# Optimization experiments

Hardware: AMD Instinct MI355X
Metric: run time of the kernel (lower is better)

The kernel has to match this reference:

```python
import jax, jax.numpy as jnp
import numpy as np

N_NODES = 100000
N_EDGES = 1600000
IN_CH = 128
HID = 128
OUT_CH = 16
N_GRAPHS = 64


def setup_inputs() -> dict:
    key = jax.random.key(0)
    ks = jax.random.split(key, 8)
    x = jax.random.normal(ks[0], (N_NODES, IN_CH), dtype=jnp.float32)
    edge_index = jax.random.randint(ks[1], (2, N_EDGES), 0, N_NODES, dtype=jnp.int64)
    batch = jnp.sort(jax.random.randint(ks[2], (N_NODES,), 0, N_GRAPHS, dtype=jnp.int64))
    s1 = 1.0 / np.sqrt(IN_CH)
    s2 = 1.0 / np.sqrt(HID)
    W1 = jax.random.uniform(ks[3], (IN_CH, HID), jnp.float32, -s1, s1)
    b1 = jnp.zeros((HID,), jnp.float32)
    W2 = jax.random.uniform(ks[4], (HID, HID), jnp.float32, -s2, s2)
    b2 = jnp.zeros((HID,), jnp.float32)
    Wfc = jax.random.uniform(ks[5], (HID, OUT_CH), jnp.float32, -s2, s2)
    bfc = jax.random.uniform(ks[6], (OUT_CH,), jnp.float32, -s2, s2)
    return {"x": x, "W1": W1, "b1": b1, "W2": W2, "b2": b2,
            "Wfc": Wfc, "bfc": bfc, "edge_index": edge_index, "batch": batch}


def _gcn_conv(x, W, b, src, dst, deg_inv_sqrt, deg_inv):
    # GCNConv with self-loops: out = D^-1/2 (A+I) D^-1/2 (x W) + b
    h = x @ W                                   # [N, H]
    norm = deg_inv_sqrt[src] * deg_inv_sqrt[dst]  # [E]
    agg = jax.ops.segment_sum(h[src] * norm[:, None], dst, num_segments=N_NODES)
    # self-loop term: deg_inv_sqrt[i]^2 * h[i]
    return agg + h * deg_inv[:, None] + b


def reference(x, W1, b1, W2, b2, Wfc, bfc, edge_index, batch):
    src, dst = edge_index[0], edge_index[1]
    # degree including self-loop
    deg = jax.ops.segment_sum(jnp.ones((N_EDGES,), jnp.float32), dst, num_segments=N_NODES) + 1.0
    deg_inv_sqrt = jax.lax.rsqrt(deg)
    deg_inv = 1.0 / deg
    h = jax.nn.relu(_gcn_conv(x, W1, b1, src, dst, deg_inv_sqrt, deg_inv))
    h = jax.nn.relu(_gcn_conv(h, W2, b2, src, dst, deg_inv_sqrt, deg_inv))
    # global mean pool over graphs
    sums = jax.ops.segment_sum(h, batch, num_segments=N_GRAPHS)          # [G, H]
    counts = jax.ops.segment_sum(jnp.ones((N_NODES,), jnp.float32), batch, num_segments=N_GRAPHS)
    pooled = sums / jnp.maximum(counts, 1.0)[:, None]
    return pooled @ Wfc + bfc
```

## Files before the change

kernel.cpp:

```cpp
#include <hip/hip_runtime.h>
#include <math.h>

#define NN 100000
#define NE 1600000
#define CH 128
#define OUTC 16
#define NG 64

#define CBSH 9
#define NCB 196
#define CHK 8192
#define MAXB 12288
#define PS 8

typedef __attribute__((ext_vector_type(8))) short bf16x8;
typedef __attribute__((ext_vector_type(4))) float f32x4;

__device__ __forceinline__ unsigned short f2bf(float f) {
    union { float f; unsigned u; } v; v.f = f;
    unsigned r = v.u + 0x7FFF + ((v.u >> 16) & 1);
    return (unsigned short)(r >> 16);
}
__device__ __forceinline__ float bflo(unsigned u) {
    union { unsigned u; float f; } v; v.u = u << 16; return v.f;
}
__device__ __forceinline__ float bfhi(unsigned u) {
    union { unsigned u; float f; } v; v.u = u & 0xffff0000u; return v.f;
}

__global__ void k_init0(int* __restrict__ bcnt) {
    int i = blockIdx.x * 256 + threadIdx.x;
    if (i < NCB) bcnt[i] = 0;
}

__global__ __launch_bounds__(1024) void k_hist(const int* __restrict__ dst, int* __restrict__ bcnt) {
    __shared__ int h[NCB];
    int t = threadIdx.x;
    if (t < NCB) h[t] = 0;
    __syncthreads();
    int base = blockIdx.x * CHK;
#pragma unroll
    for (int i = 0; i < 8; i++) {
        int e = base + i * 1024 + t;
        if (e < NE) atomicAdd(&h[dst[e] >> CBSH], 1);
    }
    __syncthreads();
    if (t < NCB && h[t]) atomicAdd(&bcnt[t], h[t]);
}

__global__ __launch_bounds__(1024) void k_bscan(const int* __restrict__ bcnt, int* __restrict__ ebase,
                        int* __restrict__ gfill, float* __restrict__ pooled) {
    __shared__ int s[256];
    int t = threadIdx.x;
    if (t < 256) s[t] = (t < NCB) ? bcnt[t] : 0;
    __syncthreads();
    for (int off = 1; off < 256; off <<= 1) {
        int v = 0;
        if (t < 256 && t >= off) v = s[t - off];
        __syncthreads();
        if (t < 256) s[t] += v;
        __syncthreads();
    }
    if (t == 0) ebase[0] = 0;
    if (t < NCB) { ebase[t + 1] = s[t]; gfill[t] = 0; }
    for (int i = t; i < NG * CH; i += 1024) pooled[i] = 0.f;
}

__global__ __launch_bounds__(1024) void k_passA(const int* __restrict__ src, const int* __restrict__ dst,
                        const int* __restrict__ ebase, int* __restrict__ gfill,
                        unsigned* __restrict__ ebuf) {
    __shared__ unsigned lbuf[CHK];
    __shared__ int hcnt[NCB];
    __shared__ int hbase[256];
    __shared__ int goff[NCB];
    int t = threadIdx.x;
    if (t < NCB) hcnt[t] = 0;
    __syncthreads();
    int base = blockIdx.x * CHK;
    int cb[8], slot[8]; unsigned pk[8];
#pragma unroll
    for (int i = 0; i < 8; i++) {
        int e = base + i * 1024 + t;
        cb[i] = -1;
        if (e < NE) {
            int d = dst[e], s = src[e];
            cb[i] = d >> CBSH;
            pk[i] = ((unsigned)s << CBSH) | (unsigned)(d & 511);
            slot[i] = atomicAdd(&hcnt[cb[i]], 1);
        }
    }
    __syncthreads();
    if (t < 256) hbase[t] = (t < NCB) ? hcnt[t] : 0;
    __syncthreads();
    for (int off = 1; off < 256; off <<= 1) {
        int v = 0;
        if (t < 256 && t >= off) v = hbase[t - off];
        __syncthreads();
        if (t < 256) hbase[t] += v;
        __syncthreads();
    }
    if (t < NCB) {
        int c = hcnt[t];
        int g = c ? atomicAdd(&gfill[t], c) : 0;
        goff[t] = ebase[t] + g - (hbase[t] - c);
    }
    __syncthreads();
#pragma unroll
    for (int i = 0; i < 8; i++) {
        if (cb[i] >= 0) lbuf[hbase[cb[i]] - hcnt[cb[i]] + slot[i]] = pk[i];
    }
    __syncthreads();
    int total = min(NE - base, CHK);
    for (int p = t; p < total; p += 1024) {
        unsigned v = lbuf[p];
        int lo = 0, hi = NCB - 1;
        while (lo < hi) { int mid = (lo + hi) >> 1; if (hbase[mid] > p) hi = mid; else lo = mid + 1; }
        ebuf[goff[lo] + p] = v;
    }
}

__global__ __launch_bounds__(1024) void k_passB(const unsigned* __restrict__ ebuf, const int* __restrict__ ebase,
                        int* __restrict__ degi, int* __restrict__ rowst,
                        float* __restrict__ dis, int* __restrict__ csr) {
    __shared__ int cnt[512];
    __shared__ int nbase[512];
    __shared__ int fill[512];
    __shared__ int stage[MAXB];
    int t = threadIdx.x;
    int cb = blockIdx.x;
    int nb0 = cb << CBSH;
    int ncnt = min(512, NN - nb0);
    int e0 = ebase[cb], e1 = ebase[cb + 1];
    if (t < 512) { cnt[t] = 0; fill[t] = 0; }
    __syncthreads();
    for (int e = e0 + t; e < e1; e += 1024)
        atomicAdd(&cnt[ebuf[e] & 511], 1);
    __syncthreads();
    if (t < 512) nbase[t] = cnt[t];
    __syncthreads();
    for (int off = 1; off < 512; off <<= 1) {
        int v = 0;
        if (t < 512 && t >= off) v = nbase[t - off];
        __syncthreads();
        if (t < 512) nbase[t] += v;
        __syncthreads();
    }
    for (int e = e0 + t; e < e1; e += 1024) {
        unsigned v = ebuf[e];
        int local = v & 511;
        int s = atomicAdd(&fill[local], 1);
        stage[nbase[local] - cnt[local] + s] = (int)(v >> CBSH);
    }
    __syncthreads();
    int total = e1 - e0;
    for (int p = t; p < total; p += 1024) csr[e0 + p] = stage[p];
    if (t < ncnt) {
        int c = cnt[t];
        degi[nb0 + t] = c;
        rowst[nb0 + t] = e0 + nbase[t] - c;
        dis[nb0 + t] = rsqrtf((float)c + 1.0f);
    }
}

__global__ void k_gptr(const int* __restrict__ batch, int* __restrict__ gptr) {
    int n = blockIdx.x * 256 + threadIdx.x;
    if (n >= NN) return;
    int b = batch[n];
    int prev = (n == 0) ? -1 : batch[n - 1];
    for (int g = prev + 1; g <= b; g++) gptr[g] = n;
    if (n == NN - 1) {
        for (int g = b + 1; g <= NG; g++) gptr[g] = NN;
    }
}

__global__ void k_castW(const float* __restrict__ W1, const float* __restrict__ W2,
                        unsigned short* __restrict__ wt1, unsigned short* __restrict__ wt2) {
    int i = blockIdx.x * 256 + threadIdx.x;
    if (i < CH * CH) {
        int k = i >> 7, n = i & 127;
        wt1[n * CH + k] = f2bf(W1[i]);
    } else if (i < 2 * CH * CH) {
        int j = i - CH * CH;
        int k = j >> 7, n = j & 127;
        wt2[n * CH + k] = f2bf(W2[j]);
    }
}

template<bool F32IN>
__launch_bounds__(256, 2)
__global__ void k_gemm(const void* __restrict__ Av,
                       const unsigned short* __restrict__ WT,
                       const float* __restrict__ dis,
                       unsigned short* __restrict__ out) {
    int tid = threadIdx.x;
    int wave = tid >> 6, lane = tid & 63;
    int quad = lane >> 4, l16 = lane & 15;

    int rbase = blockIdx.x * 128 + wave * 32;

    bf16x8 af[2][4];
#pragma unroll
    for (int s = 0; s < 2; s++) {
        int row = rbase + s * 16 + l16;
        if (row >= NN) row = NN - 1;
        if (F32IN) {
            const float* arow = (const float*)Av + (size_t)row * CH + quad * 8;
#pragma unroll
            for (int ks = 0; ks < 4; ks++) {
                float4 lo = *(const float4*)(arow + ks * 32);
                float4 hi = *(const float4*)(arow + ks * 32 + 4);
                union { bf16x8 v; unsigned short u[8]; } tmp;
                tmp.u[0] = f2bf(lo.x); tmp.u[1] = f2bf(lo.y);
                tmp.u[2] = f2bf(lo.z); tmp.u[3] = f2bf(lo.w);
                tmp.u[4] = f2bf(hi.x); tmp.u[5] = f2bf(hi.y);
                tmp.u[6] = f2bf(hi.z); tmp.u[7] = f2bf(hi.w);
                af[s][ks] = tmp.v;
            }
        } else {
            const unsigned short* arow = (const unsigned short*)Av + (size_t)row * CH + quad * 8;
#pragma unroll
            for (int ks = 0; ks < 4; ks++) af[s][ks] = *(const bf16x8*)(arow + ks * 32);
        }
    }

    f32x4 acc[2][8];
#pragma unroll
    for (int s = 0; s < 2; s++)
#pragma unroll
        for (int t = 0; t < 8; t++) acc[s][t] = (f32x4){0.f, 0.f, 0.f, 0.f};

#pragma unroll
    for (int t = 0; t < 8; t++) {
        const unsigned short* wcol = WT + (size_t)(t * 16 + l16) * CH + quad * 8;
        bf16x8 b0 = *(const bf16x8*)(wcol);
        bf16x8 b1 = *(const bf16x8*)(wcol + 32);
        bf16x8 b2 = *(const bf16x8*)(wcol + 64);
        bf16x8 b3 = *(const bf16x8*)(wcol + 96);
#pragma unroll
        for (int s = 0; s < 2; s++) {
            acc[s][t] = __builtin_amdgcn_mfma_f32_16x16x32_bf16(af[s][0], b0, acc[s][t], 0, 0, 0);
            acc[s][t] = __builtin_amdgcn_mfma_f32_16x16x32_bf16(af[s][1], b1, acc[s][t], 0, 0, 0);
            acc[s][t] = __builtin_amdgcn_mfma_f32_16x16x32_bf16(af[s][2], b2, acc[s][t], 0, 0, 0);
            acc[s][t] = __builtin_amdgcn_mfma_f32_16x16x32_bf16(af[s][3], b3, acc[s][t], 0, 0, 0);
        }
    }

#pragma unroll
    for (int s = 0; s < 2; s++) {
#pragma unroll
        for (int r = 0; r < 4; r++) {
            int orow = rbase + s * 16 + quad * 4 + r;
            if (orow < NN) {
                float d = dis[orow];
#pragma unroll
                for (int t = 0; t < 8; t++) {
                    out[(size_t)orow * CH + t * 16 + l16] = f2bf(acc[s][t][r] * d);
                }
            }
        }
    }
}

__global__ void k_agg(const unsigned short* __restrict__ ht, const int* __restrict__ rowst,
                      const int* __restrict__ degi, const int* __restrict__ csr,
                      const float* __restrict__ dis, const float* __restrict__ bias,
                      unsigned short* __restrict__ out) {
    int wave = threadIdx.x >> 6;
    int lane = threadIdx.x & 63;
    int n = blockIdx.x * 4 + wave;
    if (n >= NN) return;
    const unsigned* base = (const unsigned*)ht;
    unsigned sv = base[(size_t)n * 64 + lane];
    float a0[8], a1[8];
    a0[0] = bflo(sv); a1[0] = bfhi(sv);
#pragma unroll
    for (int u = 1; u < 8; u++) { a0[u] = 0.f; a1[u] = 0.f; }
    int start = __builtin_amdgcn_readfirstlane(rowst[n]);
    int c = __builtin_amdgcn_readfirstlane(degi[n]);
    int j = 0;
    for (; j + 7 < c; j += 8) {
        int idx[8];
#pragma unroll
        for (int u = 0; u < 8; u++) idx[u] = csr[start + j + u];
        unsigned v[8];
#pragma unroll
        for (int u = 0; u < 8; u++) v[u] = base[(size_t)idx[u] * 64 + lane];
#pragma unroll
        for (int u = 0; u < 8; u++) { a0[u] += bflo(v[u]); a1[u] += bfhi(v[u]); }
    }
    for (; j < c; j++) {
        unsigned v0 = base[(size_t)csr[start + j] * 64 + lane];
        a0[j & 7] += bflo(v0); a1[j & 7] += bfhi(v0);
    }
#pragma unroll
    for (int off = 4; off >= 1; off >>= 1)
#pragma unroll
        for (int u = 0; u < off; u++) { a0[u] += a0[u + off]; a1[u] += a1[u + off]; }
    float d = dis[n];
    float bb0 = bias[lane * 2], bb1 = bias[lane * 2 + 1];
    float ox = fmaxf(fmaf(d, a0[0], bb0), 0.f);
    float oy = fmaxf(fmaf(d, a1[0], bb1), 0.f);
    unsigned pk = ((unsigned)f2bf(oy) << 16) | (unsigned)f2bf(ox);
    ((unsigned*)out)[(size_t)n * 64 + lane] = pk;
}

__global__ __launch_bounds__(512) void k_pool2(const unsigned short* __restrict__ h,
                                               const int* __restrict__ gptr,
                                               float* __restrict__ pooled) {
    int g = blockIdx.x >> 3;
    int s = blockIdx.x & 7;
    int gs = gptr[g], ge = gptr[g + 1];
    int len = ge - gs;
    int i0 = gs + (int)(((long long)len * s) >> 3);
    int i1 = gs + (int)(((long long)len * (s + 1)) >> 3);
    int t = threadIdx.x;
    int pr = t & 63;
    int ro = t >> 6;
    const unsigned* base = (const unsigned*)h;
    float s0 = 0.f, s1 = 0.f;
    for (int n = i0 + ro; n < i1; n += 8) {
        unsigned v = base[(size_t)n * 64 + pr];
        s0 += bflo(v); s1 += bfhi(v);
    }
    __shared__ float red[2][8][64];
    red[0][ro][pr] = s0; red[1][ro][pr] = s1;
    __syncthreads();
    for (int off = 4; off >= 1; off >>= 1) {
        if (ro < off) {
            red[0][ro][pr] += red[0][ro + off][pr];
            red[1][ro][pr] += red[1][ro + off][pr];
        }
        __syncthreads();
    }
    if (ro == 0) {
        atomicAdd(&pooled[g * CH + pr * 2],     red[0][0][pr]);
        atomicAdd(&pooled[g * CH + pr * 2 + 1], red[1][0][pr]);
    }
}

__global__ void k_final(const float* __restrict__ pooled, const int* __restrict__ gptr,
                        const float* __restrict__ Wfc, const float* __restrict__ bfc,
                        float* __restrict__ out) {
    int idx = blockIdx.x * 256 + threadIdx.x;
    if (idx >= NG * OUTC) return;
    int g = idx >> 4, o = idx & 15;
    float c = (float)(gptr[g + 1] - gptr[g]);
    float inv = 1.0f / fmaxf(c, 1.0f);
    float s = 0.f;
    for (int k = 0; k < CH; k++) s += pooled[g * CH + k] * Wfc[k * OUTC + o];
    out[idx] = fmaf(s, inv, bfc[o]);
}

extern "C" void kernel_launch(void* const* d_in, const int* in_sizes, int n_in,
                              void* d_out, int out_size, void* d_ws, size_t ws_size,
                              hipStream_t stream) {
    (void)in_sizes; (void)n_in; (void)out_size; (void)ws_size;
    const float* x   = (const float*)d_in[0];
    const float* W1  = (const float*)d_in[1];
    const float* b1  = (const float*)d_in[2];
    const float* W2  = (const float*)d_in[3];
    const float* b2  = (const float*)d_in[4];
    const float* Wfc = (const float*)d_in[5];
    const float* bfc = (const float*)d_in[6];
    const int* ei    = (const int*)d_in[7];
    const int* batch = (const int*)d_in[8];
    const int* esrc = ei;
    const int* edst = ei + NE;
    float* out = (float*)d_out;

    char* w = (char*)d_ws;
    unsigned short* bufA = (unsigned short*)w; w += (size_t)NN * CH * 2;
    unsigned short* bufB = (unsigned short*)w; w += (size_t)NN * CH * 2;
    unsigned short* wt1  = (unsigned short*)w; w += (size_t)CH * CH * 2;
    unsigned short* wt2  = (unsigned short*)w; w += (size_t)CH * CH * 2;
    unsigned* ebuf = (unsigned*)w; w += (size_t)NE * 4;
    int* csr    = (int*)w;    w += (size_t)NE * 4;
    int* degi   = (int*)w;    w += (size_t)NN * 4;
    int* rowst  = (int*)w;    w += (size_t)NN * 4;
    float* dis  = (float*)w;  w += (size_t)NN * 4;
    int* bcnt   = (int*)w;    w += NCB * 4;
    int* ebase  = (int*)w;    w += (NCB + 1) * 4;
    int* gfill  = (int*)w;    w += NCB * 4;
    int* gptr   = (int*)w;    w += (NG + 1) * 4;
    float* pooled = (float*)w; w += (size_t)NG * CH * 4;

    const int histBlocks = (NE + CHK - 1) / CHK;
    const int gemmBlocks = (NN + 127) / 128;

    k_init0<<<1, 256, 0, stream>>>(bcnt);
    k_hist<<<histBlocks, 1024, 0, stream>>>(edst, bcnt);
    k_bscan<<<1, 1024, 0, stream>>>(bcnt, ebase, gfill, pooled);
    k_passA<<<histBlocks, 1024, 0, stream>>>(esrc, edst, ebase, gfill, ebuf);
    k_passB<<<NCB, 1024, 0, stream>>>(ebuf, ebase, degi, rowst, dis, csr);
    k_gptr<<<(NN + 255) / 256, 256, 0, stream>>>(batch, gptr);

    k_castW<<<(2 * CH * CH + 255) / 256, 256, 0, stream>>>(W1, W2, wt1, wt2);

    k_gemm<true><<<gemmBlocks, 256, 0, stream>>>(x, wt1, dis, bufA);
    k_agg<<<NN / 4, 256, 0, stream>>>(bufA, rowst, degi, csr, dis, b1, bufB);
    k_gemm<false><<<gemmBlocks, 256, 0, stream>>>(bufB, wt2, dis, bufA);
    k_agg<<<NN / 4, 256, 0, stream>>>(bufA, rowst, degi, csr, dis, b2, bufB);

    k_pool2<<<NG * PS, 512, 0, stream>>>(bufB, gptr, pooled);
    k_final<<<(NG * OUTC + 255) / 256, 256, 0, stream>>>(pooled, gptr, Wfc, bfc, out);
}
```

Measured before the change: 334.0 us.

## Fuse prep kernels, store bucket ids in passA, scalarize agg index loads

```diff
diff --git a/kernel.cpp b/kernel.cpp
--- a/kernel.cpp
+++ b/kernel.cpp
@@ -28,9 +28,28 @@
     union { unsigned u; float f; } v; v.u = u & 0xffff0000u; return v.f;
 }
 
-__global__ void k_init0(int* __restrict__ bcnt) {
+__global__ void k_prep(const float* __restrict__ W1, const float* __restrict__ W2,
+                       unsigned short* __restrict__ wt1, unsigned short* __restrict__ wt2,
+                       const int* __restrict__ batch, int* __restrict__ gptr,
+                       int* __restrict__ bcnt) {
     int i = blockIdx.x * 256 + threadIdx.x;
+    if (i < CH * CH) {
+        int k = i >> 7, n = i & 127;
+        wt1[n * CH + k] = f2bf(W1[i]);
+    } else if (i < 2 * CH * CH) {
+        int j = i - CH * CH;
+        int k = j >> 7, n = j & 127;
+        wt2[n * CH + k] = f2bf(W2[j]);
+    }
     if (i < NCB) bcnt[i] = 0;
+    if (i < NN) {
+        int b = batch[i];
+        int prev = (i == 0) ? -1 : batch[i - 1];
+        for (int g = prev + 1; g <= b; g++) gptr[g] = i;
+        if (i == NN - 1) {
+            for (int g = b + 1; g <= NG; g++) gptr[g] = NN;
+        }
+    }
 }
 
 __global__ __launch_bounds__(1024) void k_hist(const int* __restrict__ dst, int* __restrict__ bcnt) {
@@ -70,6 +89,7 @@
                         const int* __restrict__ ebase, int* __restrict__ gfill,
                         unsigned* __restrict__ ebuf) {
     __shared__ unsigned lbuf[CHK];
+    __shared__ unsigned char lbyte[CHK];
     __shared__ int hcnt[NCB];
     __shared__ int hbase[256];
     __shared__ int goff[NCB];
@@ -107,15 +127,18 @@
     __syncthreads();
 #pragma unroll
     for (int i = 0; i < 8; i++) {
-        if (cb[i] >= 0) lbuf[hbase[cb[i]] - hcnt[cb[i]] + slot[i]] = pk[i];
+        if (cb[i] >= 0) {
+            int pos = hbase[cb[i]] - hcnt[cb[i]] + slot[i];
+            lbuf[pos] = pk[i];
+            lbyte[pos] = (unsigned char)cb[i];
+        }
     }
     __syncthreads();
     int total = min(NE - base, CHK);
     for (int p = t; p < total; p += 1024) {
         unsigned v = lbuf[p];
-        int lo = 0, hi = NCB - 1;
-        while (lo < hi) { int mid = (lo + hi) >> 1; if (hbase[mid] > p) hi = mid; else lo = mid + 1; }
-        ebuf[goff[lo] + p] = v;
+        int b = lbyte[p];
+        ebuf[goff[b] + p] = v;
     }
 }
 
@@ -162,30 +185,6 @@
     }
 }
 
-__global__ void k_gptr(const int* __restrict__ batch, int* __restrict__ gptr) {
-    int n = blockIdx.x * 256 + threadIdx.x;
-    if (n >= NN) return;
-    int b = batch[n];
-    int prev = (n == 0) ? -1 : batch[n - 1];
-    for (int g = prev + 1; g <= b; g++) gptr[g] = n;
-    if (n == NN - 1) {
-        for (int g = b + 1; g <= NG; g++) gptr[g] = NN;
-    }
-}
-
-__global__ void k_castW(const float* __restrict__ W1, const float* __restrict__ W2,
-                        unsigned short* __restrict__ wt1, unsigned short* __restrict__ wt2) {
-    int i = blockIdx.x * 256 + threadIdx.x;
-    if (i < CH * CH) {
-        int k = i >> 7, n = i & 127;
-        wt1[n * CH + k] = f2bf(W1[i]);
-    } else if (i < 2 * CH * CH) {
-        int j = i - CH * CH;
-        int k = j >> 7, n = j & 127;
-        wt2[n * CH + k] = f2bf(W2[j]);
-    }
-}
-
 template<bool F32IN>
 __launch_bounds__(256, 2)
 __global__ void k_gemm(const void* __restrict__ Av,
@@ -279,17 +278,18 @@
     int c = __builtin_amdgcn_readfirstlane(degi[n]);
     int j = 0;
     for (; j + 7 < c; j += 8) {
-        int idx[8];
-#pragma unroll
-        for (int u = 0; u < 8; u++) idx[u] = csr[start + j + u];
         unsigned v[8];
 #pragma unroll
-        for (int u = 0; u < 8; u++) v[u] = base[(size_t)idx[u] * 64 + lane];
+        for (int u = 0; u < 8; u++) {
+            int si = __builtin_amdgcn_readfirstlane(csr[start + j + u]);
+            v[u] = base[(size_t)si * 64 + lane];
+        }
 #pragma unroll
         for (int u = 0; u < 8; u++) { a0[u] += bflo(v[u]); a1[u] += bfhi(v[u]); }
     }
     for (; j < c; j++) {
-        unsigned v0 = base[(size_t)csr[start + j] * 64 + lane];
+        int si = __builtin_amdgcn_readfirstlane(csr[start + j]);
+        unsigned v0 = base[(size_t)si * 64 + lane];
         a0[j & 7] += bflo(v0); a1[j & 7] += bfhi(v0);
     }
 #pragma unroll
@@ -387,14 +387,11 @@
     const int histBlocks = (NE + CHK - 1) / CHK;
     const int gemmBlocks = (NN + 127) / 128;
 
-    k_init0<<<1, 256, 0, stream>>>(bcnt);
+    k_prep<<<(NN + 255) / 256, 256, 0, stream>>>(W1, W2, wt1, wt2, batch, gptr, bcnt);
     k_hist<<<histBlocks, 1024, 0, stream>>>(edst, bcnt);
     k_bscan<<<1, 1024, 0, stream>>>(bcnt, ebase, gfill, pooled);
     k_passA<<<histBlocks, 1024, 0, stream>>>(esrc, edst, ebase, gfill, ebuf);
     k_passB<<<NCB, 1024, 0, stream>>>(ebuf, ebase, degi, rowst, dis, csr);
-    k_gptr<<<(NN + 255) / 256, 256, 0, stream>>>(batch, gptr);
-
-    k_castW<<<(2 * CH * CH + 255) / 256, 256, 0, stream>>>(W1, W2, wt1, wt2);
 
     k_gemm<true><<<gemmBlocks, 256, 0, stream>>>(x, wt1, dis, bufA);
     k_agg<<<NN / 4, 256, 0, stream>>>(bufA, rowst, degi, csr, dis, b1, bufB);
```

New measurement: 328.0 us. Within noise of the previous version (-1.8%).
